# Optimization experiments

Measured on AMD Instinct MI355X. Metric: run time of the kernel, lower is better.

The kernel has to match this reference:

```python
import jax, jax.numpy as jnp
import numpy as np

V = 32000          # output_dim / num_embeddings
E = 1024           # embedding_dim == hidden_size
NL = 2             # num_layers
EOS_IDX = V - 1
EPS = 1e-3
LOG_BOUND = float(np.log(1.0 - EPS))
B, T = 4, 512


def setup_inputs() -> dict:
    key = jax.random.key(0)
    ks = jax.random.split(key, 12)
    s = 1.0 / np.sqrt(E)
    inp = {
        "tokens": jax.random.randint(ks[0], (B, T), 0, V, dtype=jnp.int32),
        "emb": jax.random.normal(ks[1], (V, E), jnp.float32) * 0.02,
        "Wproj": jax.random.normal(ks[2], (V, E), jnp.float32) * 0.02,
    }
    for l in range(NL):
        inp[f"Wih{l}"] = jax.random.uniform(ks[3 + 4 * l], (4 * E, E), jnp.float32, -s, s)
        inp[f"Whh{l}"] = jax.random.uniform(ks[4 + 4 * l], (4 * E, E), jnp.float32, -s, s)
        inp[f"bih{l}"] = jax.random.uniform(ks[5 + 4 * l], (4 * E,), jnp.float32, -s, s)
        inp[f"bhh{l}"] = jax.random.uniform(ks[6 + 4 * l], (4 * E,), jnp.float32, -s, s)
    return inp


def _lstm_layer(x, Wih, Whh, bih, bhh):
    # x: [T, B, E] -> [T, B, H], PyTorch gate order i,f,g,o
    Bsz, H = x.shape[1], Whh.shape[1]
    b = bih + bhh

    def step(carry, xt):
        h, c = carry
        g = xt @ Wih.T + h @ Whh.T + b          # [B, 4H]
        i, f, gg, o = jnp.split(g, 4, axis=-1)
        c = jax.nn.sigmoid(f) * c + jax.nn.sigmoid(i) * jnp.tanh(gg)
        h = jax.nn.sigmoid(o) * jnp.tanh(c)
        return (h, c), h

    h0 = jnp.zeros((Bsz, H), x.dtype)
    _, hs = jax.lax.scan(step, (h0, h0), x)
    return hs


def _forward(tokens, emb, Wih0, Whh0, bih0, bhh0, Wih1, Whh1, bih1, bhh1, Wproj):
    x = emb[tokens]                              # [B, T, E]
    h = jnp.swapaxes(x, 0, 1)                    # [T, B, E]
    h = _lstm_layer(h, Wih0, Whh0, bih0, bhh0)
    h = _lstm_layer(h, Wih1, Whh1, bih1, bhh1)
    h_all = jnp.swapaxes(h, 0, 1)                # [B, T, E]
    logits = h_all @ Wproj.T                     # [B, T, V]

    v_lprobs = jax.nn.log_softmax(logits[..., :EOS_IDX], axis=-1)  # [B,T,V-1]
    eos_logits = logits[..., EOS_IDX:EOS_IDX + 1]                  # [B,T,1]

    # cumsum of constant log(1-eps) over time -> (t+1)*log(1-eps)
    t = jnp.arange(1, T + 1, dtype=logits.dtype)
    log_lb = (t * LOG_BOUND)[None, :, None]                        # [1,T,1]
    f_lower_bound = 1.0 - jnp.exp(log_lb)

    log_eos_ub = jax.nn.log_sigmoid(eos_logits)
    log_eos_lb = jax.nn.log_sigmoid(-eos_logits)

    v_lprobs = log_lb + log_eos_lb + v_lprobs
    log_lb_eos = jnp.log(f_lower_bound) + log_eos_lb
    # log(a+b) = log(a) - log(sigmoid(log(a) - log(b)))
    lprob_eos = log_lb_eos - jax.nn.log_sigmoid(log_lb_eos - log_eos_ub)

    log_ps = jnp.concatenate([v_lprobs, lprob_eos], axis=-1)       # [B,T,V]
    log_ps = log_ps - jax.nn.logsumexp(log_ps, axis=-1, keepdims=True)
    return log_ps


def reference(tokens, emb, Wih0, Whh0, bih0, bhh0, Wih1, Whh1, bih1, bhh1, Wproj):
    return _forward(tokens, emb, Wih0, Whh0, bih0, bhh0, Wih1, Whh1, bih1, bhh1, Wproj)
```

## Files before the change

### kernel.cpp

```cpp
#include <hip/hip_runtime.h>
#include <cstddef>

#define BB 4
#define TT 512
#define EE 1024
#define G4 4096
#define VV 32000
#define EOSI 31999
#define LOG_BOUND (-1.0005003335835335e-3f)

__device__ __forceinline__ float softplusf(float x) {
  return fmaxf(x, 0.0f) + log1pf(expf(-fabsf(x)));
}
__device__ __forceinline__ float sigmoidf(float x) {
  return 1.0f / (1.0f + expf(-x));
}

__global__ void init_state(float* h0, float* h1, float* c0, float* c1) {
  int i = blockIdx.x * 256 + threadIdx.x;
  h0[i] = 0.f; h1[i] = 0.f; c0[i] = 0.f; c1[i] = 0.f;
}

__global__ __launch_bounds__(256) void gemm_nt(
    const float* __restrict__ A, const float* __restrict__ Bw,
    float* __restrict__ C, int M, int N, int K,
    const float* __restrict__ bias1, const float* __restrict__ bias2,
    const int* __restrict__ tokens, int mode)
{
  __shared__ float As[16][132];
  __shared__ float Bs[16][132];
  const int tid  = threadIdx.x;
  const int bcol = blockIdx.x * 128;
  const int brow = blockIdx.y * 128;

  const int idx0 = tid, idx1 = tid + 256;
  const int ar0 = idx0 >> 2, ak0 = (idx0 & 3) * 4;
  const int ar1 = idx1 >> 2, ak1 = (idx1 & 3) * 4;

  long arow0, arow1;
  {
    int m0 = brow + ar0, m1 = brow + ar1;
    if (mode == 1) {
      arow0 = tokens[((m0 & 3) << 9) + (m0 >> 2)];
      arow1 = tokens[((m1 & 3) << 9) + (m1 >> 2)];
    } else if (mode == 2) {
      arow0 = ((m0 & 511) << 2) + (m0 >> 9) + 4;
      arow1 = ((m1 & 511) << 2) + (m1 >> 9) + 4;
    } else {
      arow0 = m0; arow1 = m1;
    }
  }
  const long brw0 = bcol + ar0, brw1 = bcol + ar1;

  float acc[8][8];
  #pragma unroll
  for (int i = 0; i < 8; ++i)
    #pragma unroll
    for (int j = 0; j < 8; ++j) acc[i][j] = 0.f;

  const int ti = tid >> 4, tj = tid & 15;

  for (int k0 = 0; k0 < K; k0 += 16) {
    float4 a0 = *(const float4*)(A  + arow0 * (long)K + k0 + ak0);
    float4 a1 = *(const float4*)(A  + arow1 * (long)K + k0 + ak1);
    float4 b0 = *(const float4*)(Bw + brw0  * (long)K + k0 + ak0);
    float4 b1 = *(const float4*)(Bw + brw1  * (long)K + k0 + ak1);
    __syncthreads();
    As[ak0+0][ar0] = a0.x; As[ak0+1][ar0] = a0.y; As[ak0+2][ar0] = a0.z; As[ak0+3][ar0] = a0.w;
    As[ak1+0][ar1] = a1.x; As[ak1+1][ar1] = a1.y; As[ak1+2][ar1] = a1.z; As[ak1+3][ar1] = a1.w;
    Bs[ak0+0][ar0] = b0.x; Bs[ak0+1][ar0] = b0.y; Bs[ak0+2][ar0] = b0.z; Bs[ak0+3][ar0] = b0.w;
    Bs[ak1+0][ar1] = b1.x; Bs[ak1+1][ar1] = b1.y; Bs[ak1+2][ar1] = b1.z; Bs[ak1+3][ar1] = b1.w;
    __syncthreads();
    #pragma unroll
    for (int kk = 0; kk < 16; ++kk) {
      float af[8], bf[8];
      #pragma unroll
      for (int i = 0; i < 8; ++i) af[i] = As[kk][ti*8 + i];
      #pragma unroll
      for (int j = 0; j < 8; ++j) bf[j] = Bs[kk][tj*8 + j];
      #pragma unroll
      for (int i = 0; i < 8; ++i)
        #pragma unroll
        for (int j = 0; j < 8; ++j) acc[i][j] += af[i] * bf[j];
    }
  }

  float bv[8];
  #pragma unroll
  for (int jj = 0; jj < 8; ++jj) {
    int n = bcol + tj*8 + jj;
    float bb = 0.f;
    if (bias1) bb += bias1[n];
    if (bias2) bb += bias2[n];
    bv[jj] = bb;
  }
  #pragma unroll
  for (int i = 0; i < 8; ++i) {
    int m = brow + ti*8 + i;
    float* cp = C + (size_t)m * N + bcol + tj*8;
    float4 v0 = make_float4(acc[i][0]+bv[0], acc[i][1]+bv[1], acc[i][2]+bv[2], acc[i][3]+bv[3]);
    float4 v1 = make_float4(acc[i][4]+bv[4], acc[i][5]+bv[5], acc[i][6]+bv[6], acc[i][7]+bv[7]);
    *(float4*)cp = v0;
    *(float4*)(cp + 4) = v1;
  }
}

__global__ __launch_bounds__(256) void lstm_step(
    const float* __restrict__ gpre,
    const float* __restrict__ Whh,
    const float* __restrict__ hprev,
    float* __restrict__ hout,
    float* __restrict__ cst)
{
  __shared__ float hs[4 * 1024];
  __shared__ float part[32][8][4];
  __shared__ float gv[32][4];
  const int tid = threadIdx.x;

  {
    const float4* hp4 = (const float4*)hprev;
    float4* hw = (float4*)hs;
    for (int i = tid; i < 1024; i += 256) hw[i] = hp4[i];
  }
  __syncthreads();

  const int rl = tid >> 3, ks = tid & 7;
  const int gate = rl >> 3, jl = rl & 7;
  const int j = blockIdx.x * 8 + jl;
  const int grow = gate * 1024 + j;
  const float4* w4 = (const float4*)(Whh + (size_t)grow * 1024);
  const float4* h4 = (const float4*)hs;

  float a0 = 0.f, a1 = 0.f, a2 = 0.f, a3 = 0.f;
  #pragma unroll 4
  for (int i = 0; i < 32; ++i) {
    int k4 = i * 8 + ks;
    float4 w  = w4[k4];
    float4 h0 = h4[k4];
    float4 h1 = h4[256 + k4];
    float4 h2 = h4[512 + k4];
    float4 h3 = h4[768 + k4];
    a0 += w.x*h0.x + w.y*h0.y + w.z*h0.z + w.w*h0.w;
    a1 += w.x*h1.x + w.y*h1.y + w.z*h1.z + w.w*h1.w;
    a2 += w.x*h2.x + w.y*h2.y + w.z*h2.z + w.w*h2.w;
    a3 += w.x*h3.x + w.y*h3.y + w.z*h3.z + w.w*h3.w;
  }
  *(float4*)&part[rl][ks][0] = make_float4(a0, a1, a2, a3);
  __syncthreads();

  if (tid < 128) {
    int r = tid >> 2, b = tid & 3;
    float s = 0.f;
    #pragma unroll
    for (int k = 0; k < 8; ++k) s += part[r][k][b];
    int gr = (r >> 3) * 1024 + blockIdx.x * 8 + (r & 7);
    gv[r][b] = gpre[b * 4096 + gr] + s;
  }
  __syncthreads();

  if (tid < 32) {
    int jj = tid >> 2, b = tid & 3;
    float gi = gv[jj][b], gf = gv[8 + jj][b], gg = gv[16 + jj][b], go = gv[24 + jj][b];
    int o = b * 1024 + blockIdx.x * 8 + jj;
    float c = sigmoidf(gf) * cst[o] + sigmoidf(gi) * tanhf(gg);
    cst[o] = c;
    hout[o] = sigmoidf(go) * tanhf(c);
  }
}

__global__ __launch_bounds__(256) void row_stats(
    const float* __restrict__ logits, float* __restrict__ rowA, float* __restrict__ rowE)
{
  const int m = blockIdx.x;
  const float* row = logits + (size_t)m * VV;
  __shared__ float red[8];
  const int tid = threadIdx.x;

  float mx = -3.0e38f;
  for (int v = tid; v < EOSI; v += 256) mx = fmaxf(mx, row[v]);
  for (int off = 32; off; off >>= 1) mx = fmaxf(mx, __shfl_down(mx, off, 64));
  if ((tid & 63) == 0) red[tid >> 6] = mx;
  __syncthreads();
  if (tid == 0) red[4] = fmaxf(fmaxf(red[0], red[1]), fmaxf(red[2], red[3]));
  __syncthreads();
  mx = red[4];

  float s = 0.f;
  for (int v = tid; v < EOSI; v += 256) s += expf(row[v] - mx);
  for (int off = 32; off; off >>= 1) s += __shfl_down(s, off, 64);
  if ((tid & 63) == 0) red[tid >> 6] = s;
  __syncthreads();

  if (tid == 0) {
    s = red[0] + red[1] + red[2] + red[3];
    float lse_v = mx + logf(s);
    float eos = row[EOSI];
    int t = m & 511;
    float log_lb = (float)(t + 1) * LOG_BOUND;
    float log_eos_lb = -softplusf(eos);
    float log_eos_ub = -softplusf(-eos);
    float shift = log_lb + log_eos_lb;
    float f_lb = -expm1f(log_lb);
    float log_lb_eos = logf(f_lb) + log_eos_lb;
    float lprob_eos = log_lb_eos + softplusf(log_eos_ub - log_lb_eos);
    float aa = shift, bb = lprob_eos;
    float lse2 = fmaxf(aa, bb) + log1pf(expf(-fabsf(aa - bb)));
    rowA[m] = lse_v + lse2 - shift;
    rowE[m] = lprob_eos - lse2;
  }
}

__global__ __launch_bounds__(256) void finalize(
    float* __restrict__ out, const float* __restrict__ rowA, const float* __restrict__ rowE)
{
  const int m = blockIdx.y;
  const int v4 = blockIdx.x * 256 + threadIdx.x;
  if (v4 >= 8000) return;
  float4* rp = (float4*)(out + (size_t)m * VV);
  const float A = rowA[m];
  float4 p = rp[v4];
  p.x -= A; p.y -= A; p.z -= A; p.w -= A;
  if (v4 == 7999) p.w = rowE[m];
  rp[v4] = p;
}

extern "C" void kernel_launch(void* const* d_in, const int* in_sizes, int n_in,
                              void* d_out, int out_size, void* d_ws, size_t ws_size,
                              hipStream_t stream)
{
  const int*   tokens = (const int*)  d_in[0];
  const float* emb    = (const float*)d_in[1];
  const float* Wproj  = (const float*)d_in[2];
  const float* Wih0   = (const float*)d_in[3];
  const float* Whh0   = (const float*)d_in[4];
  const float* bih0   = (const float*)d_in[5];
  const float* bhh0   = (const float*)d_in[6];
  const float* Wih1   = (const float*)d_in[7];
  const float* Whh1   = (const float*)d_in[8];
  const float* bih1   = (const float*)d_in[9];
  const float* bhh1   = (const float*)d_in[10];
  float* out = (float*)d_out;

  float* ws = (float*)d_ws;
  float* g0   = ws;
  float* g1   = g0 + (size_t)2048*4096;
  float* h0   = g1 + (size_t)2048*4096;
  float* h1   = h0 + (size_t)513*4096;
  float* c0   = h1 + (size_t)513*4096;
  float* c1   = c0 + 4096;
  float* rowA = c1 + 4096;
  float* rowE = rowA + 2048;

  init_state<<<16, 256, 0, stream>>>(h0, h1, c0, c1);

  gemm_nt<<<dim3(32, 16), 256, 0, stream>>>(emb, Wih0, g0, 2048, 4096, 1024,
                                            bih0, bhh0, tokens, 1);
  for (int t = 0; t < 512; ++t)
    lstm_step<<<128, 256, 0, stream>>>(g0 + (size_t)t*4*4096, Whh0,
                                       h0 + (size_t)t*4096, h0 + (size_t)(t+1)*4096, c0);

  gemm_nt<<<dim3(32, 16), 256, 0, stream>>>(h0 + 4096, Wih1, g1, 2048, 4096, 1024,
                                            bih1, bhh1, nullptr, 0);
  for (int t = 0; t < 512; ++t)
    lstm_step<<<128, 256, 0, stream>>>(g1 + (size_t)t*4*4096, Whh1,
                                       h1 + (size_t)t*4096, h1 + (size_t)(t+1)*4096, c1);

  gemm_nt<<<dim3(250, 16), 256, 0, stream>>>(h1, Wproj, out, 2048, 32000, 1024,
                                             nullptr, nullptr, nullptr, 2);

  row_stats<<<2048, 256, 0, stream>>>(out, rowA, rowE);
  finalize<<<dim3(32, 2048), 256, 0, stream>>>(out, rowA, rowE);
}
```

Baseline: 9.289 ms.

## Use bf16 MFMA GEMMs and persistent LSTM kernel with grid barrier

The three large GEMMs now convert fp32 tiles to bf16 in shared memory and use 16x16x32 bf16 MFMA instructions instead of scalar fp32 FMA. The 1024 per-step LSTM launches are replaced by one persistent kernel per layer. It keeps each block's Whh slice in registers and the cell state in a register, and synchronises timesteps with a global atomic barrier. This removes launch overhead and repeated weight reads, but it lowers GEMM precision to bf16 and depends on all 256 blocks being co-resident for the spin barrier.

```diff
diff --git a/kernel.cpp b/kernel.cpp
--- a/kernel.cpp
+++ b/kernel.cpp
@@ -1,170 +1,206 @@
 #include <hip/hip_runtime.h>
 #include <cstddef>
 
-#define BB 4
-#define TT 512
-#define EE 1024
-#define G4 4096
 #define VV 32000
 #define EOSI 31999
 #define LOG_BOUND (-1.0005003335835335e-3f)
 
+typedef float  floatx4  __attribute__((ext_vector_type(4)));
+typedef short  bf16x8   __attribute__((ext_vector_type(8)));
+typedef unsigned short ushortx8 __attribute__((ext_vector_type(8)));
+
 __device__ __forceinline__ float softplusf(float x) {
   return fmaxf(x, 0.0f) + log1pf(expf(-fabsf(x)));
 }
 __device__ __forceinline__ float sigmoidf(float x) {
   return 1.0f / (1.0f + expf(-x));
 }
-
-__global__ void init_state(float* h0, float* h1, float* c0, float* c1) {
+__device__ __forceinline__ unsigned short f2bf(float f) {
+  union { float f; unsigned u; } v; v.f = f;
+  unsigned u = v.u;
+  return (unsigned short)((u + 0x7fffu + ((u >> 16) & 1u)) >> 16);
+}
+
+__global__ void init_misc(float* h0, float* h1, unsigned* bars) {
   int i = blockIdx.x * 256 + threadIdx.x;
-  h0[i] = 0.f; h1[i] = 0.f; c0[i] = 0.f; c1[i] = 0.f;
-}
-
-__global__ __launch_bounds__(256) void gemm_nt(
-    const float* __restrict__ A, const float* __restrict__ Bw,
-    float* __restrict__ C, int M, int N, int K,
+  h0[i] = 0.f; h1[i] = 0.f;
+  if (i < 8) bars[i] = 0u;
+}
+
+__global__ __launch_bounds__(256) void mgemm(
+    const float* __restrict__ A, const float* __restrict__ B, float* __restrict__ C,
+    int M, int N, int K,
     const float* __restrict__ bias1, const float* __restrict__ bias2,
-    const int* __restrict__ tokens, int mode)
-{
-  __shared__ float As[16][132];
-  __shared__ float Bs[16][132];
+    const int* __restrict__ tokens, int mode, int arow_off)
+{
+  __shared__ unsigned short As[128 * 40];
+  __shared__ unsigned short Bs[128 * 40];
+
   const int tid  = threadIdx.x;
-  const int bcol = blockIdx.x * 128;
-  const int brow = blockIdx.y * 128;
-
-  const int idx0 = tid, idx1 = tid + 256;
-  const int ar0 = idx0 >> 2, ak0 = (idx0 & 3) * 4;
-  const int ar1 = idx1 >> 2, ak1 = (idx1 & 3) * 4;
-
-  long arow0, arow1;
+  const int wave = tid >> 6, lane = tid & 63;
+  const int ln15 = lane & 15, kq = lane >> 4;
+  const int bcol = blockIdx.x * 128, brow = blockIdx.y * 128;
+  const int wm = (wave >> 1) * 64, wn = (wave & 1) * 64;
+
+  const int sr = tid >> 1, sh = (tid & 1) * 16;
+  long arow;
   {
-    int m0 = brow + ar0, m1 = brow + ar1;
-    if (mode == 1) {
-      arow0 = tokens[((m0 & 3) << 9) + (m0 >> 2)];
-      arow1 = tokens[((m1 & 3) << 9) + (m1 >> 2)];
-    } else if (mode == 2) {
-      arow0 = ((m0 & 511) << 2) + (m0 >> 9) + 4;
-      arow1 = ((m1 & 511) << 2) + (m1 >> 9) + 4;
-    } else {
-      arow0 = m0; arow1 = m1;
-    }
-  }
-  const long brw0 = bcol + ar0, brw1 = bcol + ar1;
-
-  float acc[8][8];
+    int m = brow + sr;
+    if (mode == 1)      arow = tokens[((m & 3) << 9) + (m >> 2)];
+    else if (mode == 2) arow = ((m & 511) << 2) + (m >> 9) + 4;
+    else                arow = m + arow_off;
+  }
+  const float* Ap = A + arow * (long)K + sh;
+  const float* Bp = B + (long)(bcol + sr) * K + sh;
+
+  floatx4 acc[4][4];
   #pragma unroll
-  for (int i = 0; i < 8; ++i)
-    #pragma unroll
-    for (int j = 0; j < 8; ++j) acc[i][j] = 0.f;
-
-  const int ti = tid >> 4, tj = tid & 15;
-
-  for (int k0 = 0; k0 < K; k0 += 16) {
-    float4 a0 = *(const float4*)(A  + arow0 * (long)K + k0 + ak0);
-    float4 a1 = *(const float4*)(A  + arow1 * (long)K + k0 + ak1);
-    float4 b0 = *(const float4*)(Bw + brw0  * (long)K + k0 + ak0);
-    float4 b1 = *(const float4*)(Bw + brw1  * (long)K + k0 + ak1);
-    __syncthreads();
-    As[ak0+0][ar0] = a0.x; As[ak0+1][ar0] = a0.y; As[ak0+2][ar0] = a0.z; As[ak0+3][ar0] = a0.w;
-    As[ak1+0][ar1] = a1.x; As[ak1+1][ar1] = a1.y; As[ak1+2][ar1] = a1.z; As[ak1+3][ar1] = a1.w;
-    Bs[ak0+0][ar0] = b0.x; Bs[ak0+1][ar0] = b0.y; Bs[ak0+2][ar0] = b0.z; Bs[ak0+3][ar0] = b0.w;
-    Bs[ak1+0][ar1] = b1.x; Bs[ak1+1][ar1] = b1.y; Bs[ak1+2][ar1] = b1.z; Bs[ak1+3][ar1] = b1.w;
-    __syncthreads();
-    #pragma unroll
-    for (int kk = 0; kk < 16; ++kk) {
-      float af[8], bf[8];
+  for (int i = 0; i < 4; ++i)
+    #pragma unroll
+    for (int j = 0; j < 4; ++j)
+      acc[i][j] = (floatx4){0.f, 0.f, 0.f, 0.f};
+
+  for (int k0 = 0; k0 < K; k0 += 32) {
+    float4 a0 = *(const float4*)(Ap + k0 + 0);
+    float4 a1 = *(const float4*)(Ap + k0 + 4);
+    float4 a2 = *(const float4*)(Ap + k0 + 8);
+    float4 a3 = *(const float4*)(Ap + k0 + 12);
+    float4 b0 = *(const float4*)(Bp + k0 + 0);
+    float4 b1 = *(const float4*)(Bp + k0 + 4);
+    float4 b2 = *(const float4*)(Bp + k0 + 8);
+    float4 b3 = *(const float4*)(Bp + k0 + 12);
+    __syncthreads();
+    {
+      ushortx8 p0, p1;
+      p0[0]=f2bf(a0.x); p0[1]=f2bf(a0.y); p0[2]=f2bf(a0.z); p0[3]=f2bf(a0.w);
+      p0[4]=f2bf(a1.x); p0[5]=f2bf(a1.y); p0[6]=f2bf(a1.z); p0[7]=f2bf(a1.w);
+      p1[0]=f2bf(a2.x); p1[1]=f2bf(a2.y); p1[2]=f2bf(a2.z); p1[3]=f2bf(a2.w);
+      p1[4]=f2bf(a3.x); p1[5]=f2bf(a3.y); p1[6]=f2bf(a3.z); p1[7]=f2bf(a3.w);
+      *(ushortx8*)&As[sr * 40 + sh]     = p0;
+      *(ushortx8*)&As[sr * 40 + sh + 8] = p1;
+      p0[0]=f2bf(b0.x); p0[1]=f2bf(b0.y); p0[2]=f2bf(b0.z); p0[3]=f2bf(b0.w);
+      p0[4]=f2bf(b1.x); p0[5]=f2bf(b1.y); p0[6]=f2bf(b1.z); p0[7]=f2bf(b1.w);
+      p1[0]=f2bf(b2.x); p1[1]=f2bf(b2.y); p1[2]=f2bf(b2.z); p1[3]=f2bf(b2.w);
+      p1[4]=f2bf(b3.x); p1[5]=f2bf(b3.y); p1[6]=f2bf(b3.z); p1[7]=f2bf(b3.w);
+      *(ushortx8*)&Bs[sr * 40 + sh]     = p0;
+      *(ushortx8*)&Bs[sr * 40 + sh + 8] = p1;
+    }
+    __syncthreads();
+
+    bf16x8 af[4], bfr[4];
+    #pragma unroll
+    for (int i = 0; i < 4; ++i)
+      af[i] = *(const bf16x8*)&As[(wm + i * 16 + ln15) * 40 + kq * 8];
+    #pragma unroll
+    for (int j = 0; j < 4; ++j)
+      bfr[j] = *(const bf16x8*)&Bs[(wn + j * 16 + ln15) * 40 + kq * 8];
+    #pragma unroll
+    for (int i = 0; i < 4; ++i)
       #pragma unroll
-      for (int i = 0; i < 8; ++i) af[i] = As[kk][ti*8 + i];
+      for (int j = 0; j < 4; ++j)
+        acc[i][j] = __builtin_amdgcn_mfma_f32_16x16x32_bf16(af[i], bfr[j], acc[i][j], 0, 0, 0);
+  }
+
+  #pragma unroll
+  for (int j = 0; j < 4; ++j) {
+    int col = bcol + wn + j * 16 + ln15;
+    float bb = bias1 ? (bias1[col] + bias2[col]) : 0.f;
+    #pragma unroll
+    for (int i = 0; i < 4; ++i) {
+      int row0 = brow + wm + i * 16 + kq * 4;
       #pragma unroll
-      for (int j = 0; j < 8; ++j) bf[j] = Bs[kk][tj*8 + j];
-      #pragma unroll
-      for (int i = 0; i < 8; ++i)
-        #pragma unroll
-        for (int j = 0; j < 8; ++j) acc[i][j] += af[i] * bf[j];
-    }
-  }
-
-  float bv[8];
-  #pragma unroll
-  for (int jj = 0; jj < 8; ++jj) {
-    int n = bcol + tj*8 + jj;
-    float bb = 0.f;
-    if (bias1) bb += bias1[n];
-    if (bias2) bb += bias2[n];
-    bv[jj] = bb;
-  }
-  #pragma unroll
-  for (int i = 0; i < 8; ++i) {
-    int m = brow + ti*8 + i;
-    float* cp = C + (size_t)m * N + bcol + tj*8;
-    float4 v0 = make_float4(acc[i][0]+bv[0], acc[i][1]+bv[1], acc[i][2]+bv[2], acc[i][3]+bv[3]);
-    float4 v1 = make_float4(acc[i][4]+bv[4], acc[i][5]+bv[5], acc[i][6]+bv[6], acc[i][7]+bv[7]);
-    *(float4*)cp = v0;
-    *(float4*)(cp + 4) = v1;
-  }
-}
-
-__global__ __launch_bounds__(256) void lstm_step(
+      for (int r = 0; r < 4; ++r)
+        C[(size_t)(row0 + r) * N + col] = acc[i][j][r] + bb;
+    }
+  }
+}
+
+__global__ __launch_bounds__(256) void lstm_persist(
     const float* __restrict__ gpre,
     const float* __restrict__ Whh,
-    const float* __restrict__ hprev,
-    float* __restrict__ hout,
-    float* __restrict__ cst)
-{
-  __shared__ float hs[4 * 1024];
-  __shared__ float part[32][8][4];
-  __shared__ float gv[32][4];
+    float* __restrict__ hbuf,
+    unsigned* __restrict__ bar)
+{
+  __shared__ float hs[4096];
+  __shared__ float part[16][17][4];
+  __shared__ float gv[16][4];
+
   const int tid = threadIdx.x;
-
+  const int bl  = blockIdx.x;
+  const int row = tid >> 4, ks = tid & 15;
+  const int wrow = (row >> 2) * 1024 + bl * 4 + (row & 3);
+
+  float4 wreg[16];
   {
-    const float4* hp4 = (const float4*)hprev;
-    float4* hw = (float4*)hs;
-    for (int i = tid; i < 1024; i += 256) hw[i] = hp4[i];
-  }
-  __syncthreads();
-
-  const int rl = tid >> 3, ks = tid & 7;
-  const int gate = rl >> 3, jl = rl & 7;
-  const int j = blockIdx.x * 8 + jl;
-  const int grow = gate * 1024 + j;
-  const float4* w4 = (const float4*)(Whh + (size_t)grow * 1024);
-  const float4* h4 = (const float4*)hs;
-
-  float a0 = 0.f, a1 = 0.f, a2 = 0.f, a3 = 0.f;
-  #pragma unroll 4
-  for (int i = 0; i < 32; ++i) {
-    int k4 = i * 8 + ks;
-    float4 w  = w4[k4];
-    float4 h0 = h4[k4];
-    float4 h1 = h4[256 + k4];
-    float4 h2 = h4[512 + k4];
-    float4 h3 = h4[768 + k4];
-    a0 += w.x*h0.x + w.y*h0.y + w.z*h0.z + w.w*h0.w;
-    a1 += w.x*h1.x + w.y*h1.y + w.z*h1.z + w.w*h1.w;
-    a2 += w.x*h2.x + w.y*h2.y + w.z*h2.z + w.w*h2.w;
-    a3 += w.x*h3.x + w.y*h3.y + w.z*h3.z + w.w*h3.w;
-  }
-  *(float4*)&part[rl][ks][0] = make_float4(a0, a1, a2, a3);
-  __syncthreads();
-
-  if (tid < 128) {
-    int r = tid >> 2, b = tid & 3;
-    float s = 0.f;
-    #pragma unroll
-    for (int k = 0; k < 8; ++k) s += part[r][k][b];
-    int gr = (r >> 3) * 1024 + blockIdx.x * 8 + (r & 7);
-    gv[r][b] = gpre[b * 4096 + gr] + s;
-  }
-  __syncthreads();
-
-  if (tid < 32) {
-    int jj = tid >> 2, b = tid & 3;
-    float gi = gv[jj][b], gf = gv[8 + jj][b], gg = gv[16 + jj][b], go = gv[24 + jj][b];
-    int o = b * 1024 + blockIdx.x * 8 + jj;
-    float c = sigmoidf(gf) * cst[o] + sigmoidf(gi) * tanhf(gg);
-    cst[o] = c;
-    hout[o] = sigmoidf(go) * tanhf(c);
+    const float4* w4 = (const float4*)(Whh + (size_t)wrow * 1024);
+    #pragma unroll
+    for (int i = 0; i < 16; ++i) wreg[i] = w4[i * 16 + ks];
+  }
+
+  const int rb_r = tid >> 2, rb_b = tid & 3;
+  const int g_d  = tid >> 2, g_b  = tid & 3;
+  float creg = 0.f;
+
+  for (int t = 0; t < 512; ++t) {
+    float gp = 0.f;
+    if (tid < 64)
+      gp = gpre[(size_t)(t * 4 + rb_b) * 4096 + (rb_r >> 2) * 1024 + bl * 4 + (rb_r & 3)];
+
+    {
+      const float4* hp = (const float4*)(hbuf + (size_t)t * 4096);
+      float4* hsv = (float4*)hs;
+      #pragma unroll
+      for (int i = 0; i < 4; ++i) hsv[tid + i * 256] = hp[tid + i * 256];
+    }
+    __syncthreads();
+
+    const float4* h4 = (const float4*)hs;
+    float a0 = 0.f, a1 = 0.f, a2 = 0.f, a3 = 0.f;
+    #pragma unroll
+    for (int i = 0; i < 16; ++i) {
+      int k4 = i * 16 + ks;
+      float4 w  = wreg[i];
+      float4 h0 = h4[k4];
+      float4 h1 = h4[256 + k4];
+      float4 h2 = h4[512 + k4];
+      float4 h3 = h4[768 + k4];
+      a0 += w.x*h0.x + w.y*h0.y + w.z*h0.z + w.w*h0.w;
+      a1 += w.x*h1.x + w.y*h1.y + w.z*h1.z + w.w*h1.w;
+      a2 += w.x*h2.x + w.y*h2.y + w.z*h2.z + w.w*h2.w;
+      a3 += w.x*h3.x + w.y*h3.y + w.z*h3.z + w.w*h3.w;
+    }
+    *(float4*)&part[row][ks][0] = make_float4(a0, a1, a2, a3);
+    __syncthreads();
+
+    if (tid < 64) {
+      float s = 0.f;
+      #pragma unroll
+      for (int k = 0; k < 16; ++k) s += part[rb_r][k][rb_b];
+      gv[rb_r][rb_b] = gp + s;
+    }
+    __syncthreads();
+
+    if (tid < 16) {
+      float gi = gv[g_d][g_b], gf = gv[4 + g_d][g_b];
+      float gg = gv[8 + g_d][g_b], go = gv[12 + g_d][g_b];
+      float c = sigmoidf(gf) * creg + sigmoidf(gi) * tanhf(gg);
+      creg = c;
+      float h = sigmoidf(go) * tanhf(c);
+      hbuf[(size_t)(t + 1) * 4096 + g_b * 1024 + bl * 4 + g_d] = h;
+    }
+    __syncthreads();
+
+    if (t < 511) {
+      if (tid == 0) {
+        __threadfence();
+        __hip_atomic_fetch_add(bar, 1u, __ATOMIC_RELEASE, __HIP_MEMORY_SCOPE_AGENT);
+        unsigned tgt = 256u * (unsigned)(t + 1);
+        while (__hip_atomic_load(bar, __ATOMIC_ACQUIRE, __HIP_MEMORY_SCOPE_AGENT) < tgt) {
+          __builtin_amdgcn_s_sleep(1);
+        }
+      }
+      __syncthreads();
+    }
   }
 }
 
@@ -172,12 +208,12 @@
     const float* __restrict__ logits, float* __restrict__ rowA, float* __restrict__ rowE)
 {
   const int m = blockIdx.x;
-  const float* row = logits + (size_t)m * VV;
+  const float* rowp = logits + (size_t)m * VV;
   __shared__ float red[8];
   const int tid = threadIdx.x;
 
   float mx = -3.0e38f;
-  for (int v = tid; v < EOSI; v += 256) mx = fmaxf(mx, row[v]);
+  for (int v = tid; v < EOSI; v += 256) mx = fmaxf(mx, rowp[v]);
   for (int off = 32; off; off >>= 1) mx = fmaxf(mx, __shfl_down(mx, off, 64));
   if ((tid & 63) == 0) red[tid >> 6] = mx;
   __syncthreads();
@@ -186,7 +222,7 @@
   mx = red[4];
 
   float s = 0.f;
-  for (int v = tid; v < EOSI; v += 256) s += expf(row[v] - mx);
+  for (int v = tid; v < EOSI; v += 256) s += expf(rowp[v] - mx);
   for (int off = 32; off; off >>= 1) s += __shfl_down(s, off, 64);
   if ((tid & 63) == 0) red[tid >> 6] = s;
   __syncthreads();
@@ -194,7 +230,7 @@
   if (tid == 0) {
     s = red[0] + red[1] + red[2] + red[3];
     float lse_v = mx + logf(s);
-    float eos = row[EOSI];
+    float eos = rowp[EOSI];
     int t = m & 511;
     float log_lb = (float)(t + 1) * LOG_BOUND;
     float log_eos_lb = -softplusf(eos);
@@ -217,9 +253,9 @@
   const int v4 = blockIdx.x * 256 + threadIdx.x;
   if (v4 >= 8000) return;
   float4* rp = (float4*)(out + (size_t)m * VV);
-  const float A = rowA[m];
+  const float Av = rowA[m];
   float4 p = rp[v4];
-  p.x -= A; p.y -= A; p.z -= A; p.w -= A;
+  p.x -= Av; p.y -= Av; p.z -= Av; p.w -= Av;
   if (v4 == 7999) p.w = rowE[m];
   rp[v4] = p;
 }
@@ -241,32 +277,26 @@
   const float* bhh1   = (const float*)d_in[10];
   float* out = (float*)d_out;
 
-  float* ws = (float*)d_ws;
-  float* g0   = ws;
-  float* g1   = g0 + (size_t)2048*4096;
-  float* h0   = g1 + (size_t)2048*4096;
-  float* h1   = h0 + (size_t)513*4096;
-  float* c0   = h1 + (size_t)513*4096;
-  float* c1   = c0 + 4096;
-  float* rowA = c1 + 4096;
+  float* ws   = (float*)d_ws;
+  float* g    = ws;
+  float* h0   = g  + (size_t)2048 * 4096;
+  float* h1   = h0 + (size_t)513 * 4096;
+  float* rowA = h1 + (size_t)513 * 4096;
   float* rowE = rowA + 2048;
-
-  init_state<<<16, 256, 0, stream>>>(h0, h1, c0, c1);
-
-  gemm_nt<<<dim3(32, 16), 256, 0, stream>>>(emb, Wih0, g0, 2048, 4096, 1024,
-                                            bih0, bhh0, tokens, 1);
-  for (int t = 0; t < 512; ++t)
-    lstm_step<<<128, 256, 0, stream>>>(g0 + (size_t)t*4*4096, Whh0,
-                                       h0 + (size_t)t*4096, h0 + (size_t)(t+1)*4096, c0);
-
-  gemm_nt<<<dim3(32, 16), 256, 0, stream>>>(h0 + 4096, Wih1, g1, 2048, 4096, 1024,
-                                            bih1, bhh1, nullptr, 0);
-  for (int t = 0; t < 512; ++t)
-    lstm_step<<<128, 256, 0, stream>>>(g1 + (size_t)t*4*4096, Whh1,
-                                       h1 + (size_t)t*4096, h1 + (size_t)(t+1)*4096, c1);
-
-  gemm_nt<<<dim3(250, 16), 256, 0, stream>>>(h1, Wproj, out, 2048, 32000, 1024,
-                                             nullptr, nullptr, nullptr, 2);
+  unsigned* bars = (unsigned*)(rowE + 2048);
+
+  init_misc<<<16, 256, 0, stream>>>(h0, h1, bars);
+
+  mgemm<<<dim3(32, 16), 256, 0, stream>>>(emb, Wih0, g, 2048, 4096, 1024,
+                                          bih0, bhh0, tokens, 1, 0);
+  lstm_persist<<<256, 256, 0, stream>>>(g, Whh0, h0, bars + 0);
+
+  mgemm<<<dim3(32, 16), 256, 0, stream>>>(h0, Wih1, g, 2048, 4096, 1024,
+                                          bih1, bhh1, nullptr, 0, 4);
+  lstm_persist<<<256, 256, 0, stream>>>(g, Whh1, h1, bars + 1);
+
+  mgemm<<<dim3(250, 16), 256, 0, stream>>>(h1, Wproj, out, 2048, 32000, 1024,
+                                           nullptr, nullptr, nullptr, 2, 0);
 
   row_stats<<<2048, 256, 0, stream>>>(out, rowA, rowE);
   finalize<<<dim3(32, 2048), 256, 0, stream>>>(out, rowA, rowE);
```

Measured after the change: 17.50 ms. 88.4% more time.
